# Kernel tuning notes

Measured on AMD Instinct MI355X. Metric: run time of the kernel, lower is better.

The kernel has to match this reference:

```python
import jax, jax.numpy as jnp
import numpy as np

B, S, HID, NH = 4, 1024, 1024, 16
HD = HID // NH  # 64


def setup_inputs() -> dict:
    key = jax.random.key(0)
    ks = jax.random.split(key, 8)
    scale = 0.02
    return {
        "attention_mask": jnp.zeros((B, 1, 1, S), dtype=jnp.float32),
        "query": jax.random.normal(ks[0], (B, S, HID), dtype=jnp.float32),
        "key": jax.random.normal(ks[1], (B, S, HID), dtype=jnp.float32),
        "value": jax.random.normal(ks[2], (B, S, HID), dtype=jnp.float32),
        "Wq": jax.random.normal(ks[3], (HID, HID), dtype=jnp.float32) * scale,
        "bq": jnp.zeros((HID,), dtype=jnp.float32),
        "Wk": jax.random.normal(ks[4], (HID, HID), dtype=jnp.float32) * scale,
        "bk": jnp.zeros((HID,), dtype=jnp.float32),
    }


def reference(attention_mask, query, key, value, Wq, bq, Wk, bk):
    # Linear projections (torch Linear: x @ W.T + b)
    q = query @ Wq.T + bq  # [B,S,HID]
    k = key @ Wk.T + bk    # [B,S,HID]
    # split heads -> [B,NH,S,HD]
    q = q.reshape(B, S, NH, HD).transpose(0, 2, 1, 3)
    k = k.reshape(B, S, NH, HD).transpose(0, 2, 1, 3)
    scores = jnp.einsum("bhqd,bhkd->bhqk", q, k) / jnp.sqrt(jnp.float32(HD))
    scores = scores + attention_mask  # additive mask broadcast [B,1,1,S]
    probs = jax.nn.softmax(scores, axis=-1)  # [B,NH,S,S]
    # V is shared across heads; head-mean folds into a single contraction:
    # mean_h(probs_h @ V) = (sum_h probs_h) @ V / NH
    out = jnp.einsum("bhqk,bkv->bqv", probs, value) / NH  # [B,S,HID]
    return out
```

## Files before the change

### kernel.cpp

```cpp
#include <hip/hip_runtime.h>
#include <hip/hip_fp16.h>

#define B_    4
#define S_    1024
#define HID_  1024
#define NH_   16
#define HD_   64

#define LOG2E 1.44269504f
#define PSTR  40

typedef _Float16 half8 __attribute__((ext_vector_type(8)));
typedef float f32x4 __attribute__((ext_vector_type(4)));

__device__ __forceinline__ half8 cvt8(float4 a, float4 b) {
    half8 h;
    h[0] = (_Float16)a.x; h[1] = (_Float16)a.y;
    h[2] = (_Float16)a.z; h[3] = (_Float16)a.w;
    h[4] = (_Float16)b.x; h[5] = (_Float16)b.y;
    h[6] = (_Float16)b.z; h[7] = (_Float16)b.w;
    return h;
}

__device__ __forceinline__ float fexp2(float x) {
#if __has_builtin(__builtin_amdgcn_exp2f)
    return __builtin_amdgcn_exp2f(x);
#else
    float r;
    asm("v_exp_f32 %0, %1\n\ts_nop 0" : "=v"(r) : "v"(x));
    return r;
#endif
}

__device__ __forceinline__ void lds_barrier() {
    asm volatile("s_waitcnt lgkmcnt(0)" ::: "memory");
    __builtin_amdgcn_s_barrier();
    __builtin_amdgcn_sched_barrier(0);
}

__global__ __launch_bounds__(512) void proj_qk_f16(
    const float* __restrict__ query, const float* __restrict__ Wq,
    const float* __restrict__ bq, _Float16* __restrict__ Oq,
    const float* __restrict__ key, const float* __restrict__ Wk,
    const float* __restrict__ bk, _Float16* __restrict__ Ok)
{
    const int f  = blockIdx.x + 8 * blockIdx.y + 256 * blockIdx.z;
    const int w2 = (f & 7) * 64 + (f >> 3);
    const int bx = w2 & 7, by = (w2 >> 3) & 31, bz = w2 >> 8;

    const float* A    = bz ? key : query;
    const float* Wm   = bz ? Wk  : Wq;
    const float* bias = bz ? bk  : bq;
    _Float16* Co      = bz ? Ok  : Oq;

    __shared__ _Float16 Al[2][128 * PSTR];
    __shared__ _Float16 Bl[2][128 * PSTR];

    const int tid  = threadIdx.x;
    const int wv   = tid >> 6;
    const int lane = tid & 63;
    const int l15  = lane & 15;
    const int quad = lane >> 4;
    const int wm   = wv & 1, wn = wv >> 1;
    const int m0   = by * 128, n0 = bx * 128;
    const int sr   = tid >> 2;
    const int sc   = (tid & 3) * 8;

    const float* ap = A  + (long)(m0 + sr) * HID_ + sc;
    const float* bp = Wm + (long)(n0 + sr) * HID_ + sc;

    f32x4 acc[4][2];
#pragma unroll
    for (int i = 0; i < 4; i++)
#pragma unroll
        for (int j = 0; j < 2; j++) acc[i][j] = (f32x4){0.f, 0.f, 0.f, 0.f};

    float4 a0 = *(const float4*)ap,       a1 = *(const float4*)(ap + 4);
    float4 b0 = *(const float4*)bp,       b1 = *(const float4*)(bp + 4);
    *(half8*)&Al[0][sr * PSTR + sc] = cvt8(a0, a1);
    *(half8*)&Bl[0][sr * PSTR + sc] = cvt8(b0, b1);
    a0 = *(const float4*)(ap + 32); a1 = *(const float4*)(ap + 36);
    b0 = *(const float4*)(bp + 32); b1 = *(const float4*)(bp + 36);
    lds_barrier();

#pragma unroll 2
    for (int kt = 0; kt < HID_; kt += 32) {
        const int p = (kt >> 5) & 1;

        float4 na0 = a0, na1 = a1, nb0 = b0, nb1 = b1;
        if (kt + 64 < HID_) {
            na0 = *(const float4*)(ap + kt + 64);
            na1 = *(const float4*)(ap + kt + 68);
            nb0 = *(const float4*)(bp + kt + 64);
            nb1 = *(const float4*)(bp + kt + 68);
        }

        half8 af[4], bfm[2];
#pragma unroll
        for (int i = 0; i < 4; i++)
            af[i] = *(const half8*)(&Al[p][(wm * 64 + i * 16 + l15) * PSTR + quad * 8]);
#pragma unroll
        for (int j = 0; j < 2; j++)
            bfm[j] = *(const half8*)(&Bl[p][(wn * 32 + j * 16 + l15) * PSTR + quad * 8]);

        if (kt + 32 < HID_) {
            *(half8*)&Al[p ^ 1][sr * PSTR + sc] = cvt8(a0, a1);
            *(half8*)&Bl[p ^ 1][sr * PSTR + sc] = cvt8(b0, b1);
        }

#pragma unroll
        for (int i = 0; i < 4; i++)
#pragma unroll
            for (int j = 0; j < 2; j++)
                acc[i][j] = __builtin_amdgcn_mfma_f32_16x16x32_f16(
                    af[i], bfm[j], acc[i][j], 0, 0, 0);

        lds_barrier();
        a0 = na0; a1 = na1; b0 = nb0; b1 = nb1;
    }

    const int isQ = (bz == 0);
#pragma unroll
    for (int j = 0; j < 2; j++) {
        int col = n0 + wn * 32 + j * 16 + l15;
        float bv = bias[col];
        int h = col >> 6, d = col & 63, p = d >> 3, jj = d & 7;
#pragma unroll
        for (int i = 0; i < 4; i++) {
            int row = m0 + wm * 64 + i * 16 + quad * 4;
            int bb = row >> 10, ss = row & 1023;
            long base;
            if (isQ)
                base = ((((long)(bb * NH_ + h) * 64 + (ss >> 4)) * 8 + p) * 16
                        + (ss & 15)) * 8 + jj;
            else
                base = (((long)(bb * NH_ + h) * 8 + p) * 1024 + ss) * 8 + jj;
#pragma unroll
            for (int r = 0; r < 4; r++)
                Co[base + r * 8] = (_Float16)(acc[i][j][r] + bv);
        }
    }
}

__global__ __launch_bounds__(512) void attn_psum_f16(
    const _Float16* __restrict__ qb,
    const _Float16* __restrict__ kb,
    const float* __restrict__ mask,
    _Float16* __restrict__ P)
{
    const int f   = blockIdx.x + 64 * blockIdx.y + 256 * blockIdx.z;
    const int w2s = (f & 7) * 128 + (f >> 3);
    const int qt  = w2s & 63;
    const int b   = (w2s >> 6) & 3;
    const int hz  = w2s >> 8;

    const int q0   = qt * 16;
    const int tid  = threadIdx.x;
    const int w    = tid >> 6;
    const int lane = tid & 63;
    const int l15  = lane & 15;
    const int quad = lane >> 4;

    __shared__ float redS[2][16][8];

    const float SC = 0.125f * LOG2E;

    float mreg[8];
#pragma unroll
    for (int t = 0; t < 8; t++)
        mreg[t] = mask[b * S_ + t * 128 + w * 16 + l15] * LOG2E;

    f32x4 acc[8];
#pragma unroll
    for (int t = 0; t < 8; t++) acc[t] = (f32x4){0.f, 0.f, 0.f, 0.f};

    for (int ii = 0; ii < 4; ii++) {
        const int h = hz * 4 + ii;
        const _Float16* qh = qb + ((long)(b * NH_ + h) * 64 + qt) * 1024;
        const _Float16* kh = kb + (long)(b * NH_ + h) * 8192 * 8;

        half8 a0 = *(const half8*)(qh + quad * 128 + l15 * 8);
        half8 a1 = *(const half8*)(qh + (quad + 4) * 128 + l15 * 8);

        f32x4 s[8];
#pragma unroll
        for (int cc = 0; cc < 8; cc++) {
            const int key = cc * 128 + w * 16 + l15;
            half8 b0 = *(const half8*)(kh + (long)quad * 8192 + key * 8);
            half8 b1 = *(const half8*)(kh + (long)(quad + 4) * 8192 + key * 8);
            f32x4 c = (f32x4){0.f, 0.f, 0.f, 0.f};
            c = __builtin_amdgcn_mfma_f32_16x16x32_f16(a0, b0, c, 0, 0, 0);
            c = __builtin_amdgcn_mfma_f32_16x16x32_f16(a1, b1, c, 0, 0, 0);
            s[cc] = c;
        }

        const int p = ii & 1;
        float sm[4] = {0.f, 0.f, 0.f, 0.f};
#pragma unroll
        for (int t = 0; t < 8; t++)
#pragma unroll
            for (int r = 0; r < 4; r++) {
                float pr = fexp2(fmaf(s[t][r], SC, mreg[t]));
                s[t][r] = pr;
                sm[r] += pr;
            }
#pragma unroll
        for (int off = 1; off < 16; off <<= 1)
#pragma unroll
            for (int r = 0; r < 4; r++) sm[r] += __shfl_xor(sm[r], off);
        if (l15 == 0)
#pragma unroll
            for (int r = 0; r < 4; r++) redS[p][quad * 4 + r][w] = sm[r];
        __syncthreads();

#pragma unroll
        for (int r = 0; r < 4; r++) {
            float4 v0 = *(float4*)&redS[p][quad * 4 + r][0];
            float4 v1 = *(float4*)&redS[p][quad * 4 + r][4];
            float tot = (v0.x + v0.y + v0.z + v0.w) + (v1.x + v1.y + v1.z + v1.w);
            float inv = 1.f / tot;
#pragma unroll
            for (int t = 0; t < 8; t++) acc[t][r] += s[t][r] * inv;
        }
    }

    _Float16* prow = P + (long)hz * ((long)B_ * S_ * S_) + (long)(b * S_ + q0) * S_;
#pragma unroll
    for (int t = 0; t < 8; t++)
#pragma unroll
        for (int r = 0; r < 4; r++) {
            int row = quad * 4 + r;
            prow[(long)row * S_ + t * 128 + w * 16 + l15] = (_Float16)acc[t][r];
        }
}

__global__ __launch_bounds__(256) void vt_combine(
    const _Float16* __restrict__ P, _Float16* __restrict__ o,
    const float* __restrict__ V, _Float16* __restrict__ Vt)
{
    __shared__ float t[32][33];
    if (blockIdx.y == 0) {
        if (blockIdx.x >= 2048) return;
        const long QS = (long)B_ * S_ * S_;
        long i = (long)(blockIdx.x * 256 + threadIdx.x) * 8;
        half8 a = *(const half8*)(P + i);
        half8 b = *(const half8*)(P + QS + i);
        half8 c = *(const half8*)(P + 2 * QS + i);
        half8 d = *(const half8*)(P + 3 * QS + i);
        half8 r;
#pragma unroll
        for (int e = 0; e < 8; e++)
            r[e] = (_Float16)((float)a[e] + (float)b[e] + (float)c[e] + (float)d[e]);
        *(half8*)(o + i) = r;
    } else {
        const int x  = blockIdx.x;
        const int b  = x >> 10;
        const int s0 = ((x >> 5) & 31) * 32;
        const int h0 = (x & 31) * 32;
        const int tx = threadIdx.x & 31, ty = threadIdx.x >> 5;
#pragma unroll
        for (int rr = 0; rr < 4; rr++) {
            int s = s0 + ty + rr * 8;
            t[ty + rr * 8][tx] = V[((long)b * S_ + s) * HID_ + h0 + tx];
        }
        __syncthreads();
#pragma unroll
        for (int rr = 0; rr < 4; rr++) {
            int h = h0 + ty + rr * 8;
            Vt[((long)b * HID_ + h) * S_ + s0 + tx] = (_Float16)t[tx][ty + rr * 8];
        }
    }
}

__global__ __launch_bounds__(256) void pv_f16(
    const _Float16* __restrict__ Pc,
    const _Float16* __restrict__ Vt,
    float* __restrict__ out)
{
    const int f   = blockIdx.x + 16 * blockIdx.y + 128 * blockIdx.z;
    const int xcd = f & 7, ii = f >> 3;
    const int bx  = ii & 15;
    const int by  = (ii >> 4) + ((xcd & 1) << 2);
    const int b   = xcd >> 1;

    const _Float16* A  = Pc + (long)b * S_ * S_;
    const _Float16* Bm = Vt + (long)b * HID_ * S_;

    __shared__ _Float16 Al[2][128 * PSTR];
    __shared__ _Float16 Bl[2][64 * PSTR];

    const int tid  = threadIdx.x;
    const int wv   = tid >> 6;
    const int lane = tid & 63;
    const int l15  = lane & 15;
    const int quad = lane >> 4;
    const int wm   = wv & 1, wn = wv >> 1;
    const int m0   = by * 128, n0 = bx * 64;
    const int sr   = tid >> 2;
    const int sc   = (tid & 3) * 8;

    const _Float16* ap0 = A  + (long)(m0 + sr) * S_ + sc;
    const _Float16* ap1 = A  + (long)(m0 + 64 + sr) * S_ + sc;
    const _Float16* bp0 = Bm + (long)(n0 + sr) * S_ + sc;

    f32x4 acc[4][2];
#pragma unroll
    for (int i = 0; i < 4; i++)
#pragma unroll
        for (int j = 0; j < 2; j++) acc[i][j] = (f32x4){0.f, 0.f, 0.f, 0.f};

    half8 ca0 = *(const half8*)(ap0);
    half8 ca1 = *(const half8*)(ap1);
    half8 cb0 = *(const half8*)(bp0);
    *(half8*)&Al[0][sr * PSTR + sc] = ca0;
    *(half8*)&Al[0][(64 + sr) * PSTR + sc] = ca1;
    *(half8*)&Bl[0][sr * PSTR + sc] = cb0;
    ca0 = *(const half8*)(ap0 + 32);
    ca1 = *(const half8*)(ap1 + 32);
    cb0 = *(const half8*)(bp0 + 32);
    lds_barrier();

#pragma unroll 2
    for (int kt = 0; kt < S_; kt += 32) {
        const int p = (kt >> 5) & 1;

        half8 na0 = ca0, na1 = ca1, nb0 = cb0;
        if (kt + 64 < S_) {
            na0 = *(const half8*)(ap0 + kt + 64);
            na1 = *(const half8*)(ap1 + kt + 64);
            nb0 = *(const half8*)(bp0 + kt + 64);
        }

        half8 af[4], bfm[2];
#pragma unroll
        for (int i = 0; i < 4; i++)
            af[i] = *(const half8*)(&Al[p][(wm * 64 + i * 16 + l15) * PSTR + quad * 8]);
#pragma unroll
        for (int j = 0; j < 2; j++)
            bfm[j] = *(const half8*)(&Bl[p][(wn * 32 + j * 16 + l15) * PSTR + quad * 8]);

        if (kt + 32 < S_) {
            *(half8*)&Al[p ^ 1][sr * PSTR + sc] = ca0;
            *(half8*)&Al[p ^ 1][(64 + sr) * PSTR + sc] = ca1;
            *(half8*)&Bl[p ^ 1][sr * PSTR + sc] = cb0;
        }

#pragma unroll
        for (int i = 0; i < 4; i++)
#pragma unroll
            for (int j = 0; j < 2; j++)
                acc[i][j] = __builtin_amdgcn_mfma_f32_16x16x32_f16(
                    af[i], bfm[j], acc[i][j], 0, 0, 0);

        lds_barrier();
        ca0 = na0; ca1 = na1; cb0 = nb0;
    }

    const float alpha = 1.f / NH_;
#pragma unroll
    for (int i = 0; i < 4; i++) {
        int row = m0 + wm * 64 + i * 16 + quad * 4;
#pragma unroll
        for (int j = 0; j < 2; j++) {
            int col = n0 + wn * 32 + j * 16 + l15;
#pragma unroll
            for (int r = 0; r < 4; r++)
                out[(long)(b * S_ + row + r) * HID_ + col] = acc[i][j][r] * alpha;
        }
    }
}

extern "C" void kernel_launch(void* const* d_in, const int* in_sizes, int n_in,
                              void* d_out, int out_size, void* d_ws, size_t ws_size,
                              hipStream_t stream)
{
    const float* mask  = (const float*)d_in[0];
    const float* query = (const float*)d_in[1];
    const float* key   = (const float*)d_in[2];
    const float* value = (const float*)d_in[3];
    const float* Wq    = (const float*)d_in[4];
    const float* bq    = (const float*)d_in[5];
    const float* Wk    = (const float*)d_in[6];
    const float* bk    = (const float*)d_in[7];
    float* out = (float*)d_out;

    char* ws = (char*)d_ws;
    const long MB = 1l << 20;
    _Float16* qbuf = (_Float16*)(ws);
    _Float16* kbuf = (_Float16*)(ws + 8 * MB);
    _Float16* Pq   = (_Float16*)(ws + 16 * MB);
    _Float16* Vt   = (_Float16*)(ws);
    _Float16* psum = (_Float16*)(ws + 8 * MB);

    proj_qk_f16<<<dim3(HID_ / 128, (B_ * S_) / 128, 2), dim3(512), 0, stream>>>(
        query, Wq, bq, qbuf, key, Wk, bk, kbuf);

    attn_psum_f16<<<dim3(S_ / 16, B_, 4), dim3(512), 0, stream>>>(
        qbuf, kbuf, mask, Pq);

    vt_combine<<<dim3(4096, 2), dim3(256), 0, stream>>>(Pq, psum, value, Vt);

    pv_f16<<<dim3(HID_ / 64, S_ / 128, B_), dim3(256), 0, stream>>>(psum, Vt, out);
}
```

Before: 196.1 us.

## Pre-cast projection inputs to fp16 and stream tiles via global_load_lds

Adds a separate cast kernel that converts query/key and Wq/Wk to fp16 in workspace. The projection GEMM then loads fp16 tiles straight into LDS with global_load_lds, switches to 256-thread blocks with 128x64 tiles, and drops the padded LDS stride. The aim is to halve GEMM global traffic and move the conversion out of the GEMM's register path. In exchange it adds a launch plus a full fp32 read and fp16 write pass, and the unpadded LDS layout may cause bank conflicts.

```diff
diff --git a/kernel.cpp b/kernel.cpp
--- a/kernel.cpp
+++ b/kernel.cpp
@@ -38,23 +38,49 @@
     __builtin_amdgcn_sched_barrier(0);
 }
 
-__global__ __launch_bounds__(512) void proj_qk_f16(
-    const float* __restrict__ query, const float* __restrict__ Wq,
-    const float* __restrict__ bq, _Float16* __restrict__ Oq,
-    const float* __restrict__ key, const float* __restrict__ Wk,
-    const float* __restrict__ bk, _Float16* __restrict__ Ok)
-{
-    const int f  = blockIdx.x + 8 * blockIdx.y + 256 * blockIdx.z;
-    const int w2 = (f & 7) * 64 + (f >> 3);
-    const int bx = w2 & 7, by = (w2 >> 3) & 31, bz = w2 >> 8;
-
-    const float* A    = bz ? key : query;
-    const float* Wm   = bz ? Wk  : Wq;
-    const float* bias = bz ? bk  : bq;
-    _Float16* Co      = bz ? Ok  : Oq;
-
-    __shared__ _Float16 Al[2][128 * PSTR];
-    __shared__ _Float16 Bl[2][128 * PSTR];
+__device__ __forceinline__ void gll16(const _Float16* g, _Float16* l) {
+    __builtin_amdgcn_global_load_lds(
+        (const __attribute__((address_space(1))) unsigned int*)g,
+        (__attribute__((address_space(3))) unsigned int*)l, 16, 0, 0);
+}
+
+__global__ __launch_bounds__(256) void cast_f16(
+    const float* __restrict__ query, const float* __restrict__ key,
+    const float* __restrict__ Wq, const float* __restrict__ Wk,
+    _Float16* __restrict__ Af16, _Float16* __restrict__ Wf16)
+{
+    const int x = blockIdx.x;
+    if (blockIdx.y == 0) {
+        long base = ((long)x * 256 + threadIdx.x) * 8;
+        const float* src = (x < 2048) ? (query + base) : (key + base - (4l << 20));
+        float4 v0 = *(const float4*)src, v1 = *(const float4*)(src + 4);
+        *(half8*)(Af16 + base) = cvt8(v0, v1);
+    } else {
+        if (x >= 1024) return;
+        long base = ((long)x * 256 + threadIdx.x) * 8;
+        const float* src = (x < 512) ? (Wq + base) : (Wk + base - (1l << 20));
+        float4 v0 = *(const float4*)src, v1 = *(const float4*)(src + 4);
+        *(half8*)(Wf16 + base) = cvt8(v0, v1);
+    }
+}
+
+__global__ __launch_bounds__(256) void proj_qk_f16(
+    const _Float16* __restrict__ Af16,
+    const _Float16* __restrict__ Wf16,
+    const float* __restrict__ bq, const float* __restrict__ bk,
+    _Float16* __restrict__ Oq, _Float16* __restrict__ Ok)
+{
+    const int f  = blockIdx.x + 16 * blockIdx.y + 512 * blockIdx.z;
+    const int w2 = (f & 7) * 128 + (f >> 3);
+    const int bx = w2 & 15, by = (w2 >> 4) & 31, bz = w2 >> 9;
+
+    const _Float16* A    = Af16 + (long)bz * 4096 * 1024;
+    const _Float16* Wm   = Wf16 + (long)bz * 1024 * 1024;
+    const float*    bias = bz ? bk : bq;
+    _Float16*       Co   = bz ? Ok : Oq;
+
+    __shared__ _Float16 Al[2][128 * 32];
+    __shared__ _Float16 Bl[2][64 * 32];
 
     const int tid  = threadIdx.x;
     const int wv   = tid >> 6;
@@ -62,12 +88,14 @@
     const int l15  = lane & 15;
     const int quad = lane >> 4;
     const int wm   = wv & 1, wn = wv >> 1;
-    const int m0   = by * 128, n0 = bx * 128;
-    const int sr   = tid >> 2;
-    const int sc   = (tid & 3) * 8;
-
-    const float* ap = A  + (long)(m0 + sr) * HID_ + sc;
-    const float* bp = Wm + (long)(n0 + sr) * HID_ + sc;
+    const int m0   = by * 128, n0 = bx * 64;
+
+    const int srA  = (lane >> 2);
+    const int scA  = (lane & 3) * 8;
+    const _Float16* gA0 = A  + (long)(m0 + wv * 16 + srA) * 1024 + scA;
+    const _Float16* gA1 = A  + (long)(m0 + 64 + wv * 16 + srA) * 1024 + scA;
+    const _Float16* gB  = Wm + (long)(n0 + wv * 16 + srA) * 1024 + scA;
+    const int ldsW = wv * 512;
 
     f32x4 acc[4][2];
 #pragma unroll
@@ -75,48 +103,37 @@
 #pragma unroll
         for (int j = 0; j < 2; j++) acc[i][j] = (f32x4){0.f, 0.f, 0.f, 0.f};
 
-    float4 a0 = *(const float4*)ap,       a1 = *(const float4*)(ap + 4);
-    float4 b0 = *(const float4*)bp,       b1 = *(const float4*)(bp + 4);
-    *(half8*)&Al[0][sr * PSTR + sc] = cvt8(a0, a1);
-    *(half8*)&Bl[0][sr * PSTR + sc] = cvt8(b0, b1);
-    a0 = *(const float4*)(ap + 32); a1 = *(const float4*)(ap + 36);
-    b0 = *(const float4*)(bp + 32); b1 = *(const float4*)(bp + 36);
-    lds_barrier();
+    gll16(gA0, &Al[0][ldsW]);
+    gll16(gA1, &Al[0][2048 + ldsW]);
+    gll16(gB,  &Bl[0][ldsW]);
+    __syncthreads();
 
 #pragma unroll 2
     for (int kt = 0; kt < HID_; kt += 32) {
         const int p = (kt >> 5) & 1;
 
-        float4 na0 = a0, na1 = a1, nb0 = b0, nb1 = b1;
-        if (kt + 64 < HID_) {
-            na0 = *(const float4*)(ap + kt + 64);
-            na1 = *(const float4*)(ap + kt + 68);
-            nb0 = *(const float4*)(bp + kt + 64);
-            nb1 = *(const float4*)(bp + kt + 68);
-        }
-
-        half8 af[4], bfm[2];
+        if (kt + 32 < HID_) {
+            gll16(gA0 + kt + 32, &Al[p ^ 1][ldsW]);
+            gll16(gA1 + kt + 32, &Al[p ^ 1][2048 + ldsW]);
+            gll16(gB  + kt + 32, &Bl[p ^ 1][ldsW]);
+        }
+
+        half8 af[4], bf[2];
 #pragma unroll
         for (int i = 0; i < 4; i++)
-            af[i] = *(const half8*)(&Al[p][(wm * 64 + i * 16 + l15) * PSTR + quad * 8]);
+            af[i] = *(const half8*)(&Al[p][(wm * 64 + i * 16 + l15) * 32 + quad * 8]);
 #pragma unroll
         for (int j = 0; j < 2; j++)
-            bfm[j] = *(const half8*)(&Bl[p][(wn * 32 + j * 16 + l15) * PSTR + quad * 8]);
-
-        if (kt + 32 < HID_) {
-            *(half8*)&Al[p ^ 1][sr * PSTR + sc] = cvt8(a0, a1);
-            *(half8*)&Bl[p ^ 1][sr * PSTR + sc] = cvt8(b0, b1);
-        }
+            bf[j] = *(const half8*)(&Bl[p][(wn * 32 + j * 16 + l15) * 32 + quad * 8]);
 
 #pragma unroll
         for (int i = 0; i < 4; i++)
 #pragma unroll
             for (int j = 0; j < 2; j++)
                 acc[i][j] = __builtin_amdgcn_mfma_f32_16x16x32_f16(
-                    af[i], bfm[j], acc[i][j], 0, 0, 0);
-
-        lds_barrier();
-        a0 = na0; a1 = na1; b0 = nb0; b1 = nb1;
+                    af[i], bf[j], acc[i][j], 0, 0, 0);
+
+        __syncthreads();
     }
 
     const int isQ = (bz == 0);
@@ -124,17 +141,17 @@
     for (int j = 0; j < 2; j++) {
         int col = n0 + wn * 32 + j * 16 + l15;
         float bv = bias[col];
-        int h = col >> 6, d = col & 63, p = d >> 3, jj = d & 7;
+        int h = col >> 6, d = col & 63, pp = d >> 3, jj = d & 7;
 #pragma unroll
         for (int i = 0; i < 4; i++) {
             int row = m0 + wm * 64 + i * 16 + quad * 4;
             int bb = row >> 10, ss = row & 1023;
             long base;
             if (isQ)
-                base = ((((long)(bb * NH_ + h) * 64 + (ss >> 4)) * 8 + p) * 16
+                base = ((((long)(bb * NH_ + h) * 64 + (ss >> 4)) * 8 + pp) * 16
                         + (ss & 15)) * 8 + jj;
             else
-                base = (((long)(bb * NH_ + h) * 8 + p) * 1024 + ss) * 8 + jj;
+                base = (((long)(bb * NH_ + h) * 8 + pp) * 1024 + ss) * 8 + jj;
 #pragma unroll
             for (int r = 0; r < 4; r++)
                 Co[base + r * 8] = (_Float16)(acc[i][j][r] + bv);
@@ -388,12 +405,17 @@
     const long MB = 1l << 20;
     _Float16* qbuf = (_Float16*)(ws);
     _Float16* kbuf = (_Float16*)(ws + 8 * MB);
+    _Float16* Af16 = (_Float16*)(ws + 16 * MB);
+    _Float16* Wf16 = (_Float16*)(ws + 32 * MB);
     _Float16* Pq   = (_Float16*)(ws + 16 * MB);
     _Float16* Vt   = (_Float16*)(ws);
     _Float16* psum = (_Float16*)(ws + 8 * MB);
 
-    proj_qk_f16<<<dim3(HID_ / 128, (B_ * S_) / 128, 2), dim3(512), 0, stream>>>(
-        query, Wq, bq, qbuf, key, Wk, bk, kbuf);
+    cast_f16<<<dim3(4096, 2), dim3(256), 0, stream>>>(
+        query, key, Wq, Wk, Af16, Wf16);
+
+    proj_qk_f16<<<dim3(16, 32, 2), dim3(256), 0, stream>>>(
+        Af16, Wf16, bq, bk, qbuf, kbuf);
 
     attn_psum_f16<<<dim3(S_ / 16, B_, 4), dim3(512), 0, stream>>>(
         qbuf, kbuf, mask, Pq);
```

Measured after the change: 196.3 us. No clear change (+0.1%).
